# Kernel optimization log

Measured on AMD Instinct MI355X. Metric: run time of the kernel, lower is better.

The kernel has to match this reference:

```python
import math
import jax, jax.numpy as jnp
import numpy as np

V = 50257; D = 768; NL = 4; NH = 12; EXP = 4; FF = 4 * D; MAXS = 1024; ITERS = 10
HD = D // NH


def layernorm(x, g, b, eps=1e-5):
    mu = jnp.mean(x, axis=-1, keepdims=True)
    var = jnp.mean((x - mu) ** 2, axis=-1, keepdims=True)
    return (x - mu) * jax.lax.rsqrt(var + eps) * g + b


def sinkhorn(logM, iters=ITERS):
    # log-space Sinkhorn -> doubly-stochastic mixing matrix
    for _ in range(iters):
        logM = logM - jax.scipy.special.logsumexp(logM, axis=-1, keepdims=True)
        logM = logM - jax.scipy.special.logsumexp(logM, axis=-2, keepdims=True)
    return jnp.exp(logM)


def mhc(x, fn, W, b, alpha):
    # x: (B,S,n,D); dynamic manifold-constrained hyper-connection mixing
    B, S, n, d = x.shape
    xf = x.reshape(B, S, n * d)
    xn = xf * jax.lax.rsqrt(jnp.mean(xf * xf, axis=-1, keepdims=True) + 1e-6)
    logits = xn @ W * alpha + b                       # (B,S,n*n+2n)
    Hm = sinkhorn(logits[..., : n * n].reshape(B, S, n, n))
    pre = jax.nn.softmax(logits[..., n * n : n * n + n], axis=-1)   # (B,S,n)
    post = jax.nn.sigmoid(logits[..., n * n + n :])                 # (B,S,n)
    y = fn(jnp.einsum('bsn,bsnd->bsd', pre, x))                     # (B,S,D)
    return jnp.einsum('bsnm,bsmd->bsnd', Hm, x) + post[..., None] * y[:, :, None, :]


def attention(x, Wqkv, Wproj):
    B, S, _ = x.shape
    q, k, v = jnp.split(x @ Wqkv, 3, axis=-1)
    q = q.reshape(B, S, NH, HD).transpose(0, 2, 1, 3)
    k = k.reshape(B, S, NH, HD).transpose(0, 2, 1, 3)
    v = v.reshape(B, S, NH, HD).transpose(0, 2, 1, 3)
    scores = jnp.einsum('bhqd,bhkd->bhqk', q, k) * (1.0 / math.sqrt(HD))
    mask = jnp.tril(jnp.ones((S, S), dtype=bool))
    scores = jnp.where(mask, scores, -jnp.inf)
    attn = jax.nn.softmax(scores, axis=-1)
    o = jnp.einsum('bhqk,bhkd->bhqd', attn, v).transpose(0, 2, 1, 3).reshape(B, S, D)
    return o @ Wproj


def forward(input_ids, tok_emb, pos_emb, ln1_g, ln1_b, ln2_g, ln2_b,
            Wqkv, Wproj, Wfc1, Wfc2, mA_W, mA_b, mA_alpha,
            mF_W, mF_b, mF_alpha, lnf_g, lnf_b):
    B, S = input_ids.shape
    x = tok_emb[input_ids] + pos_emb[:S][None]          # (B,S,D)
    x = jnp.broadcast_to(x[:, :, None, :], (B, S, EXP, D))  # expand_to_mhc
    for l in range(NL):
        attn_fn = lambda h, l=l: attention(layernorm(h, ln1_g[l], ln1_b[l]), Wqkv[l], Wproj[l])
        x = mhc(x, attn_fn, mA_W[l], mA_b[l], mA_alpha[l])
        ffn_fn = lambda h, l=l: jax.nn.gelu(layernorm(h, ln2_g[l], ln2_b[l]) @ Wfc1[l], approximate=False) @ Wfc2[l]
        x = mhc(x, ffn_fn, mF_W[l], mF_b[l], mF_alpha[l])
    x = layernorm(jnp.sum(x, axis=2), lnf_g, lnf_b)     # contract_from_mhc + ln_f
    return x @ tok_emb.T                                # tied lm_head


def setup_inputs() -> dict:
    key = jax.random.key(0)
    ks = jax.random.split(key, 10)
    std = 0.02
    n2 = EXP * EXP + 2 * EXP
    return {
        'input_ids': jax.random.randint(ks[0], (2, 1024), 0, V),
        'tok_emb': std * jax.random.normal(ks[1], (V, D), jnp.float32),
        'pos_emb': std * jax.random.normal(ks[2], (MAXS, D), jnp.float32),
        'ln1_g': jnp.ones((NL, D)), 'ln1_b': jnp.zeros((NL, D)),
        'ln2_g': jnp.ones((NL, D)), 'ln2_b': jnp.zeros((NL, D)),
        'Wqkv': std * jax.random.normal(ks[3], (NL, D, 3 * D), jnp.float32),
        'Wproj': std * jax.random.normal(ks[4], (NL, D, D), jnp.float32),
        'Wfc1': std * jax.random.normal(ks[5], (NL, D, FF), jnp.float32),
        'Wfc2': std * jax.random.normal(ks[6], (NL, FF, D), jnp.float32),
        'mA_W': std * jax.random.normal(ks[7], (NL, EXP * D, n2), jnp.float32),
        'mA_b': jnp.zeros((NL, n2)),
        'mA_alpha': 0.01 * jnp.ones((NL,)),
        'mF_W': std * jax.random.normal(ks[8], (NL, EXP * D, n2), jnp.float32),
        'mF_b': jnp.zeros((NL, n2)),
        'mF_alpha': 0.01 * jnp.ones((NL,)),
        'lnf_g': jnp.ones((D,)), 'lnf_b': jnp.zeros((D,)),
    }


def reference(input_ids, tok_emb, pos_emb, ln1_g, ln1_b, ln2_g, ln2_b,
              Wqkv, Wproj, Wfc1, Wfc2, mA_W, mA_b, mA_alpha,
              mF_W, mF_b, mF_alpha, lnf_g, lnf_b):
    return forward(input_ids, tok_emb, pos_emb, ln1_g, ln1_b, ln2_g, ln2_b,
                   Wqkv, Wproj, Wfc1, Wfc2, mA_W, mA_b, mA_alpha,
                   mF_W, mF_b, mF_alpha, lnf_g, lnf_b)
```

## Files before the change

### kernel.cpp

```cpp
#include <hip/hip_runtime.h>
#include <math.h>

constexpr int BATCH  = 2;
constexpr int SEQ    = 1024;
constexpr int DIM    = 768;
constexpr int NLAYER = 4;
constexpr int NHEAD  = 12;
constexpr int HDIM   = 64;
constexpr int NEXP   = 4;
constexpr int FFDIM  = 3072;
constexpr int VOCAB  = 50257;
constexpr int NDIM   = NEXP * DIM;
constexpr int NC     = NEXP*NEXP + 2*NEXP;
constexpr int NTOK   = BATCH * SEQ;

using bf16x8 = __attribute__((ext_vector_type(8))) __bf16;
using f32x4  = __attribute__((ext_vector_type(4))) float;
using u16x8  = __attribute__((ext_vector_type(8))) unsigned short;

__device__ inline unsigned short f2bf(float f){
  unsigned u = __builtin_bit_cast(unsigned, f);
  u += 0x7fffu + ((u >> 16) & 1u);
  return (unsigned short)(u >> 16);
}
__device__ inline bf16x8 as_bf(u16x8 v){ return __builtin_bit_cast(bf16x8, v); }

constexpr size_t SZ_X   = (size_t)NTOK * NEXP * DIM;
constexpr size_t SZ_T   = (size_t)NTOK * DIM;
constexpr size_t O_X    = 0;
constexpr size_t O_X2   = O_X  + SZ_X;
constexpr size_t O_TMP  = O_X2 + SZ_X;
constexpr size_t O_BIG  = O_TMP + SZ_T;
constexpr size_t O_LNB  = O_BIG + (size_t)NTOK*2304;
constexpr size_t O_T1B  = O_LNB + SZ_T/2;
constexpr size_t O_COEF = O_T1B + SZ_T/2;
constexpr size_t O_WT   = O_COEF + (size_t)NTOK*NC;
constexpr size_t O_LNF  = 19298688;

__device__ inline float wred_sum(float v){
#pragma unroll
  for (int m=32;m>=1;m>>=1) v += __shfl_xor(v,m);
  return v;
}

template<bool FIRST>
__global__ __launch_bounds__(256) void k_mhc(const int* __restrict__ ids,
                                             const float* __restrict__ tokf,
                                             const float* __restrict__ posf,
                                             const float* __restrict__ xin,
                                             const float* __restrict__ y,
                                             float* __restrict__ xout,
                                             const float* __restrict__ W,
                                             const float* __restrict__ bb,
                                             const float* __restrict__ alpha_p,
                                             const float* __restrict__ g,
                                             const float* __restrict__ lnb_,
                                             float* __restrict__ coef,
                                             unsigned short* __restrict__ lnout){
  const int t = blockIdx.x, tid = threadIdx.x;
  const int w = tid >> 6;
  __shared__ float wred[4], w2[4];
  __shared__ float accw[4][NC];
  __shared__ float cfl[NC];

  float xp[3][4];
  float ss = 0.f;

  if constexpr (FIRST){
    const float* te = tokf + (size_t)ids[t]*DIM;
    const float* pe = posf + (size_t)(t % SEQ)*DIM;
#pragma unroll
    for (int k=0;k<3;k++){
      int d = tid + k*256;
      float v = te[d] + pe[d];
#pragma unroll
      for (int n=0;n<4;n++){
        xp[k][n] = v;
        xout[(size_t)t*NDIM + n*DIM + d] = v;
      }
      ss += 4.f*v*v;
    }
  } else {
    float cfp[20];
    const float* cp = coef + (size_t)t*NC;
#pragma unroll
    for (int j=0;j<16;j++) cfp[j] = cp[j];
#pragma unroll
    for (int j=0;j<4;j++) cfp[16+j] = cp[20+j];
    const float* xt = xin + (size_t)t*NDIM;
#pragma unroll
    for (int k=0;k<3;k++){
      int d = tid + k*256;
      float xm[4];
#pragma unroll
      for (int m=0;m<4;m++) xm[m] = xt[m*DIM + d];
      float yv = y[(size_t)t*DIM + d];
#pragma unroll
      for (int n=0;n<4;n++){
        float o = cfp[16+n]*yv;
#pragma unroll
        for (int m=0;m<4;m++) o += cfp[n*4+m]*xm[m];
        xp[k][n] = o;
        xout[(size_t)t*NDIM + n*DIM + d] = o;
        ss += o*o;
      }
    }
  }

  ss = wred_sum(ss);
  float acc[NC];
#pragma unroll
  for (int j=0;j<NC;j++) acc[j]=0.f;
#pragma unroll
  for (int k=0;k<3;k++){
    int d = tid + k*256;
#pragma unroll
    for (int n=0;n<4;n++){
      float v = xp[k][n];
      const float* wr = W + (size_t)(n*DIM + d)*NC;
#pragma unroll
      for (int j=0;j<NC;j++) acc[j] += v*wr[j];
    }
  }
#pragma unroll
  for (int j=0;j<NC;j++){
#pragma unroll
    for (int m=32;m>=1;m>>=1) acc[j] += __shfl_xor(acc[j], m);
  }
  if ((tid&63)==0){
    wred[w] = ss;
#pragma unroll
    for (int j=0;j<NC;j++) accw[w][j] = acc[j];
  }
  __syncthreads();
  float rfac = rsqrtf((wred[0]+wred[1]+wred[2]+wred[3])/(float)NDIM + 1e-6f);

  const float alpha = alpha_p[0];
  float* cfg = coef + (size_t)t*NC;
  if (tid < 16){
    float lmv = (accw[0][tid]+accw[1][tid]+accw[2][tid]+accw[3][tid])*rfac*alpha + bb[tid];
#pragma unroll
    for (int it=0; it<10; ++it){
      float mx = fmaxf(lmv, __shfl_xor(lmv,1)); mx = fmaxf(mx, __shfl_xor(mx,2));
      float se = expf(lmv-mx); se += __shfl_xor(se,1); se += __shfl_xor(se,2);
      lmv -= mx + logf(se);
      mx = fmaxf(lmv, __shfl_xor(lmv,4)); mx = fmaxf(mx, __shfl_xor(mx,8));
      se = expf(lmv-mx); se += __shfl_xor(se,4); se += __shfl_xor(se,8);
      lmv -= mx + logf(se);
    }
    float hm = expf(lmv);
    cfl[tid] = hm;
    cfg[tid] = hm;
  } else if (tid < 24){
    cfl[tid] = (accw[0][tid]+accw[1][tid]+accw[2][tid]+accw[3][tid])*rfac*alpha + bb[tid];
  }
  __syncthreads();
  if (tid == 0){
    float l0=cfl[16], l1=cfl[17], l2=cfl[18], l3=cfl[19];
    float pm = fmaxf(fmaxf(l0,l1),fmaxf(l2,l3));
    float e0=expf(l0-pm), e1=expf(l1-pm), e2=expf(l2-pm), e3=expf(l3-pm);
    float es=e0+e1+e2+e3;
    cfl[16]=e0/es; cfl[17]=e1/es; cfl[18]=e2/es; cfl[19]=e3/es;
#pragma unroll
    for (int j=20;j<24;j++) cfl[j] = 1.f/(1.f+expf(-cfl[j]));
#pragma unroll
    for (int j=16;j<24;j++) cfg[j] = cfl[j];
  }
  __syncthreads();

  float p0=cfl[16], p1=cfl[17], p2=cfl[18], p3=cfl[19];
  float h[3], s1=0.f, s2=0.f;
#pragma unroll
  for (int k=0;k<3;k++){
    float v = p0*xp[k][0] + p1*xp[k][1] + p2*xp[k][2] + p3*xp[k][3];
    h[k]=v; s1+=v; s2+=v*v;
  }
  s1 = wred_sum(s1); s2 = wred_sum(s2);
  if ((tid&63)==0){ wred[w]=s1; w2[w]=s2; }
  __syncthreads();
  float mu  = (wred[0]+wred[1]+wred[2]+wred[3])/(float)DIM;
  float var = (w2[0]+w2[1]+w2[2]+w2[3])/(float)DIM - mu*mu;
  float inv = rsqrtf(var + 1e-5f);
#pragma unroll
  for (int k=0;k<3;k++){
    int d = tid + k*256;
    lnout[(size_t)t*DIM+d] = f2bf((h[k]-mu)*inv*g[d] + lnb_[d]);
  }
}

__global__ __launch_bounds__(256) void k_csumln(const float* __restrict__ xin,
                                                const float* __restrict__ coef,
                                                const float* __restrict__ y,
                                                const float* __restrict__ g,
                                                const float* __restrict__ bb,
                                                unsigned short* __restrict__ out){
  const int t = blockIdx.x, tid = threadIdx.x;
  const int w = tid >> 6;
  const float* cp = coef + (size_t)t*NC;
  float cs[4];
#pragma unroll
  for (int m=0;m<4;m++) cs[m] = cp[m] + cp[4+m] + cp[8+m] + cp[12+m];
  float ps = cp[20]+cp[21]+cp[22]+cp[23];
  const float* xt = xin + (size_t)t*NDIM;
  float h[3], s1=0.f, s2=0.f;
#pragma unroll
  for (int k=0;k<3;k++){
    int d = tid + k*256;
    float v = ps * y[(size_t)t*DIM + d];
#pragma unroll
    for (int m=0;m<4;m++) v += cs[m]*xt[m*DIM + d];
    h[k]=v; s1+=v; s2+=v*v;
  }
  __shared__ float r1[4], r2[4];
  s1 = wred_sum(s1); s2 = wred_sum(s2);
  if ((tid&63)==0){ r1[w]=s1; r2[w]=s2; }
  __syncthreads();
  float mu  = (r1[0]+r1[1]+r1[2]+r1[3])/(float)DIM;
  float var = (r2[0]+r2[1]+r2[2]+r2[3])/(float)DIM - mu*mu;
  float inv = rsqrtf(var + 1e-5f);
#pragma unroll
  for (int k=0;k<3;k++){
    int d = tid + k*256;
    out[(size_t)t*DIM+d] = f2bf((h[k]-mu)*inv*g[d] + bb[d]);
  }
}

__global__ __launch_bounds__(256) void k_fattn(const unsigned short* __restrict__ qkv,
                                               unsigned short* __restrict__ out){
  const int qb = gridDim.x - 1 - blockIdx.x;
  const int h = blockIdx.y, b = blockIdx.z;
  const int tid = threadIdx.x;
  const int l = tid & 63, w = tid >> 6;
  const int lr = l & 15, lh = l >> 4;
  const int qw = qb*64 + w*16;
  constexpr int LDV = 68;
  __shared__ unsigned short Vt[64*LDV];
  __shared__ unsigned short Pl[4*16*LDV];
  unsigned short* Pw = Pl + w*16*LDV;

  const unsigned short* base = qkv + (size_t)b*SEQ*2304;

  u16x8 qa[2];
  {
    const unsigned short* qp = base + (size_t)(qw + lr)*2304 + h*64 + lh*8;
    qa[0] = *(const u16x8*)qp;
    qa[1] = *(const u16x8*)(qp + 32);
  }

  f32x4 o[4];
#pragma unroll
  for (int df=0; df<4; df++) o[df] = (f32x4){0.f,0.f,0.f,0.f};
  float m_run[4], l_run[4];
#pragma unroll
  for (int r=0;r<4;r++){ m_run[r] = -1e30f; l_run[r] = 0.f; }

  const int kTiles = qb + 1;
  for (int t=0; t<kTiles; ++t){
    const int k0 = t*64;
    __syncthreads();
#pragma unroll
    for (int i=0;i<2;i++){
      int f = tid + i*256;
      int k = f >> 3;
      int d0 = (f & 7) * 8;
      u16x8 v = *(const u16x8*)(base + (size_t)(k0+k)*2304 + 1536 + h*64 + d0);
#pragma unroll
      for (int j=0;j<8;j++) Vt[(d0+j)*LDV + k] = v[j];
    }
    __syncthreads();

    f32x4 s[4];
#pragma unroll
    for (int kf=0;kf<4;kf++) s[kf] = (f32x4){0.f,0.f,0.f,0.f};
#pragma unroll
    for (int ks=0;ks<2;ks++){
#pragma unroll
      for (int kf=0;kf<4;kf++){
        u16x8 kb = *(const u16x8*)(base + (size_t)(k0 + kf*16 + lr)*2304 + 768 + h*64 + ks*32 + lh*8);
        s[kf] = __builtin_amdgcn_mfma_f32_16x16x32_bf16(as_bf(qa[ks]), as_bf(kb), s[kf], 0,0,0);
      }
    }

    float sc[4][4];
#pragma unroll
    for (int kf=0;kf<4;kf++){
      int kg = k0 + kf*16 + lr;
#pragma unroll
      for (int r=0;r<4;r++){
        int qg = qw + lh*4 + r;
        sc[kf][r] = (kg <= qg) ? s[kf][r]*0.125f : -1e30f;
      }
    }
    float mt[4];
#pragma unroll
    for (int r=0;r<4;r++)
      mt[r] = fmaxf(fmaxf(sc[0][r],sc[1][r]), fmaxf(sc[2][r],sc[3][r]));
#pragma unroll
    for (int msk=1; msk<16; msk<<=1)
#pragma unroll
      for (int r=0;r<4;r++) mt[r] = fmaxf(mt[r], __shfl_xor(mt[r], msk));
    float c[4], rs[4];
#pragma unroll
    for (int r=0;r<4;r++){
      float mn = fmaxf(m_run[r], mt[r]);
      c[r] = expf(m_run[r] - mn);
      m_run[r] = mn;
      rs[r] = 0.f;
    }
#pragma unroll
    for (int kf=0;kf<4;kf++)
#pragma unroll
      for (int r=0;r<4;r++){
        float p = expf(sc[kf][r] - m_run[r]);
        rs[r] += p;
        Pw[(lh*4+r)*LDV + kf*16 + lr] = f2bf(p);
      }
#pragma unroll
    for (int msk=1; msk<16; msk<<=1)
#pragma unroll
      for (int r=0;r<4;r++) rs[r] += __shfl_xor(rs[r], msk);
#pragma unroll
    for (int r=0;r<4;r++) l_run[r] = l_run[r]*c[r] + rs[r];
#pragma unroll
    for (int df=0;df<4;df++)
#pragma unroll
      for (int r=0;r<4;r++) o[df][r] *= c[r];

#pragma unroll
    for (int ks=0;ks<2;ks++){
      u16x8 pa = *(const u16x8*)&Pw[lr*LDV + ks*32 + lh*8];
#pragma unroll
      for (int df=0;df<4;df++){
        u16x8 vb = *(const u16x8*)&Vt[(df*16 + lr)*LDV + ks*32 + lh*8];
        o[df] = __builtin_amdgcn_mfma_f32_16x16x32_bf16(as_bf(pa), as_bf(vb), o[df], 0,0,0);
      }
    }
  }

  float inv[4];
#pragma unroll
  for (int r=0;r<4;r++) inv[r] = 1.f/l_run[r];
#pragma unroll
  for (int df=0;df<4;df++)
#pragma unroll
    for (int r=0;r<4;r++){
      int qg = qw + lh*4 + r;
      out[((size_t)b*SEQ + qg)*DIM + h*64 + df*16 + lr] = f2bf(o[df][r]*inv[r]);
    }
}

__global__ __launch_bounds__(256) void k_wtrans4(const float* __restrict__ Wq, const float* __restrict__ Wp,
                                                 const float* __restrict__ W1, const float* __restrict__ W2,
                                                 unsigned short* __restrict__ dq, unsigned short* __restrict__ dp,
                                                 unsigned short* __restrict__ d1, unsigned short* __restrict__ d2){
  int bid = blockIdx.x;
  const float* src; unsigned short* dst; int K, N, local;
  if (bid < 1728)      { src=Wq; dst=dq; K=768;  N=2304; local=bid; }
  else if (bid < 2304) { src=Wp; dst=dp; K=768;  N=768;  local=bid-1728; }
  else if (bid < 4608) { src=W1; dst=d1; K=768;  N=3072; local=bid-2304; }
  else                 { src=W2; dst=d2; K=3072; N=768;  local=bid-4608; }
  int nx = N/32;
  int n0 = (local % nx)*32, k0 = (local / nx)*32;
  __shared__ float tile[32][33];
  int tx = threadIdx.x & 31, ty = threadIdx.x >> 5;
#pragma unroll
  for (int r=0;r<32;r+=8)
    tile[ty+r][tx] = src[(size_t)(k0+ty+r)*N + n0+tx];
  __syncthreads();
#pragma unroll
  for (int r=0;r<32;r+=8)
    dst[(size_t)(n0+ty+r)*K + k0+tx] = f2bf(tile[tx][ty+r]);
}

__global__ void k_cvt(const float* __restrict__ src, unsigned short* __restrict__ dst, int n8){
  int i = blockIdx.x*blockDim.x + threadIdx.x;
  for (; i < n8; i += gridDim.x*blockDim.x){
    float4 f0 = ((const float4*)src)[i*2];
    float4 f1 = ((const float4*)src)[i*2+1];
    u16x8 v;
    v[0]=f2bf(f0.x); v[1]=f2bf(f0.y); v[2]=f2bf(f0.z); v[3]=f2bf(f0.w);
    v[4]=f2bf(f1.x); v[5]=f2bf(f1.y); v[6]=f2bf(f1.z); v[7]=f2bf(f1.w);
    ((u16x8*)dst)[i] = v;
  }
}

template<int ACT, bool OUTBF, int BMT, int BNT, bool NT>
__global__ __launch_bounds__(256) void k_mgemm(const unsigned short* __restrict__ A,
                                               const unsigned short* __restrict__ B,
                                               void* __restrict__ Cout,
                                               int M, int N, int K)
{
  constexpr int MF = BMT/32;
  constexpr int NF = BNT/32;
  __shared__ __align__(16) unsigned short Sm[(BMT+BNT)*32];
  unsigned short* As = Sm;
  unsigned short* Bs = Sm + BMT*32;
  const int tid = threadIdx.x;
  const int l = tid & 63, w = tid >> 6;
  const int wr = w >> 1, wc = w & 1;

  const int nwg  = gridDim.x * gridDim.y;
  const int flat = blockIdx.y * gridDim.x + blockIdx.x;
  const int q8   = nwg >> 3;
  const int wk   = (flat & 7) * q8 + (flat >> 3);
  const int bm = (wk % gridDim.x) * BMT;
  const int bn = (wk / gridDim.x) * BNT;

  const int srow = tid >> 2;
  const int scol = (tid & 3) * 8;

  f32x4 acc[MF][NF];
#pragma unroll
  for (int i=0;i<MF;i++)
#pragma unroll
    for (int j=0;j<NF;j++) acc[i][j] = (f32x4){0.f,0.f,0.f,0.f};

  for (int k0 = 0; k0 < K; k0 += 32){
#pragma unroll
    for (int c=0;c<BMT/64;++c){
      const unsigned short* ga = A + (size_t)(bm + c*64 + srow)*K + (k0 + scol);
      __builtin_amdgcn_global_load_lds(
          (const __attribute__((address_space(1))) void*)ga,
          (__attribute__((address_space(3))) void*)(As + c*2048 + w*512),
          16, 0, 0);
    }
#pragma unroll
    for (int c=0;c<BNT/64;++c){
      int gn = bn + c*64 + srow; if (gn >= N) gn = N-1;
      const unsigned short* gb = B + (size_t)gn*K + (k0 + scol);
      __builtin_amdgcn_global_load_lds(
          (const __attribute__((address_space(1))) void*)gb,
          (__attribute__((address_space(3))) void*)(Bs + c*2048 + w*512),
          16, 0, 0);
    }
    __syncthreads();

    bf16x8 af[MF], bfr[NF];
#pragma unroll
    for (int i=0;i<MF;i++)
      af[i]  = *(const bf16x8*)(As + ((wr*(BMT/2) + i*16 + (l&15))*32 + (l>>4)*8));
#pragma unroll
    for (int j=0;j<NF;j++)
      bfr[j] = *(const bf16x8*)(Bs + ((wc*(BNT/2) + j*16 + (l&15))*32 + (l>>4)*8));
#pragma unroll
    for (int mi=0;mi<MF;mi++)
#pragma unroll
      for (int ni=0;ni<NF;ni++)
        acc[mi][ni] = __builtin_amdgcn_mfma_f32_16x16x32_bf16(af[mi], bfr[ni], acc[mi][ni], 0,0,0);
    __syncthreads();
  }

  if constexpr (OUTBF){
#pragma unroll
    for (int mi=0;mi<MF;mi++){
      const int gm0 = bm + wr*(BMT/2) + mi*16 + (l>>4)*4;
#pragma unroll
      for (int ni=0;ni<NF;ni++){
        const int gn = bn + wc*(BNT/2) + ni*16 + (l&15);
        if (gn < N){
#pragma unroll
          for (int r=0;r<4;r++){
            float v = acc[mi][ni][r];
            if constexpr (ACT==1) v = 0.5f*v*(1.f + erff(v*0.70710678118654752f));
            ((unsigned short*)Cout)[(size_t)(gm0+r)*N + gn] = f2bf(v);
          }
        }
      }
    }
  } else {
    float* band = (float*)Sm;
#pragma unroll
    for (int b=0; b<BMT/16; ++b){
      __syncthreads();
#pragma unroll
      for (int mi=0;mi<MF;mi++){
        if (b == wr*MF + mi){
#pragma unroll
          for (int ni=0;ni<NF;ni++){
#pragma unroll
            for (int r=0;r<4;r++){
              float v = acc[mi][ni][r];
              if constexpr (ACT==1) v = 0.5f*v*(1.f + erff(v*0.70710678118654752f));
              band[((l>>4)*4+r)*BNT + wc*(BNT/2) + ni*16 + (l&15)] = v;
            }
          }
        }
      }
      __syncthreads();
      const int row0 = bm + b*16;
#pragma unroll
      for (int p=0; p<(4*BNT)/256; ++p){
        int f = tid + p*256;
        int row = f/(BNT/4), c4 = f%(BNT/4);
        f32x4 v = *(const f32x4*)&band[row*BNT + c4*4];
        float* cp = (float*)Cout + (size_t)(row0+row)*N + bn + c4*4;
        if (bn + c4*4 + 3 < N){
          if constexpr (NT) __builtin_nontemporal_store(v, (f32x4*)cp);
          else *(f32x4*)cp = v;
        } else {
#pragma unroll
          for (int j=0;j<4;j++) if (bn + c4*4 + j < N) cp[j] = v[j];
        }
      }
    }
  }
}

extern "C" void kernel_launch(void* const* d_in, const int* in_sizes, int n_in,
                              void* d_out, int out_size, void* d_ws, size_t ws_size,
                              hipStream_t stream) {
  const int*   ids   = (const int*)  d_in[0];
  const float* tok   = (const float*)d_in[1];
  const float* pos   = (const float*)d_in[2];
  const float* ln1g  = (const float*)d_in[3];
  const float* ln1b  = (const float*)d_in[4];
  const float* ln2g  = (const float*)d_in[5];
  const float* ln2b  = (const float*)d_in[6];
  const float* Wqkv  = (const float*)d_in[7];
  const float* Wproj = (const float*)d_in[8];
  const float* Wfc1  = (const float*)d_in[9];
  const float* Wfc2  = (const float*)d_in[10];
  const float* mAW   = (const float*)d_in[11];
  const float* mAb   = (const float*)d_in[12];
  const float* mAal  = (const float*)d_in[13];
  const float* mFW   = (const float*)d_in[14];
  const float* mFb   = (const float*)d_in[15];
  const float* mFal  = (const float*)d_in[16];
  const float* lnfg  = (const float*)d_in[17];
  const float* lnfb  = (const float*)d_in[18];
  float* out = (float*)d_out;

  float* ws   = (float*)d_ws;
  float* xA   = ws + O_X;
  float* xB   = ws + O_X2;
  float* tmpF = ws + O_TMP;
  unsigned short* bigBF = (unsigned short*)(ws + O_BIG);
  unsigned short* lnbf  = (unsigned short*)(ws + O_LNB);
  unsigned short* t1bf  = (unsigned short*)(ws + O_T1B);
  float* coef = ws + O_COEF;
  unsigned short* wT    = (unsigned short*)(ws + O_WT);
  unsigned short* wqkvT  = wT;
  unsigned short* wprojT = wT + (size_t)2304*768;
  unsigned short* wfc1T  = wprojT + (size_t)768*768;
  unsigned short* wfc2T  = wfc1T + (size_t)3072*768;
  unsigned short* tokbf  = (unsigned short*)(ws + O_X);
  unsigned short* lnfbf  = (unsigned short*)(ws + O_LNF);

  float* xc = xA; float* xn = xB;
  for (int l=0; l<NLAYER; l++){
    k_wtrans4<<<6912, 256, 0, stream>>>(Wqkv + (size_t)l*DIM*3*DIM, Wproj + (size_t)l*DIM*DIM,
                                        Wfc1 + (size_t)l*DIM*FFDIM, Wfc2 + (size_t)l*FFDIM*DIM,
                                        wqkvT, wprojT, wfc1T, wfc2T);
    if (l == 0){
      k_mhc<true><<<NTOK, 256, 0, stream>>>(ids, tok, pos, nullptr, nullptr, xA,
                                            mAW, mAb, mAal, ln1g, ln1b, coef, lnbf);
    } else {
      k_mhc<false><<<NTOK, 256, 0, stream>>>(nullptr, nullptr, nullptr, xc, tmpF, xn,
                                             mAW + (size_t)l*NDIM*NC, mAb + (size_t)l*NC, mAal + l,
                                             ln1g + (size_t)l*DIM, ln1b + (size_t)l*DIM, coef, lnbf);
      { float* tmp = xc; xc = xn; xn = tmp; }
    }
    k_mgemm<0,true ,64,128,false><<<dim3(32, 2304/128), 256, 0, stream>>>(lnbf, wqkvT, (void*)bigBF, NTOK, 2304, 768);
    k_fattn<<<dim3(SEQ/64, NHEAD, BATCH), 256, 0, stream>>>(bigBF, t1bf);
    k_mgemm<0,false,64,64,false><<<dim3(32, 768/64), 256, 0, stream>>>(t1bf, wprojT, tmpF, NTOK, 768, 768);

    k_mhc<false><<<NTOK, 256, 0, stream>>>(nullptr, nullptr, nullptr, xc, tmpF, xn,
                                           mFW + (size_t)l*NDIM*NC, mFb + (size_t)l*NC, mFal + l,
                                           ln2g + (size_t)l*DIM, ln2b + (size_t)l*DIM, coef, lnbf);
    { float* tmp = xc; xc = xn; xn = tmp; }
    k_mgemm<1,true ,64,128,false><<<dim3(32, 3072/128), 256, 0, stream>>>(lnbf, wfc1T, (void*)bigBF, NTOK, 3072, 768);
    k_mgemm<0,false,64,64,false><<<dim3(32, 768/64), 256, 0, stream>>>(bigBF, wfc2T, tmpF, NTOK, 768, 3072);
  }

  k_csumln<<<NTOK, 256, 0, stream>>>(xc, coef, tmpF, lnfg, lnfb, lnfbf);
  k_cvt<<<2048, 256, 0, stream>>>(tok, tokbf, (VOCAB*DIM)/8);
  k_mgemm<0,false,128,128,true><<<dim3(16, (VOCAB+127)/128), 256, 0, stream>>>(lnfbf, tokbf, out, NTOK, VOCAB, 768);
}
```

Baseline: 1.729 ms.

## Transpose QK^T MFMA so softmax rows are lane-local, pass P via shuffles

The flash-attention kernel now computes S^T by swapping the MFMA operands, so each lane holds scores for a single query row. That collapses the max and sum reductions to two cross-lane shuffles and lets each lane keep scalar running statistics. The P tile is packed to bf16 and redistributed through register shuffles instead of a per-warp LDS buffer. V transpose stores are packed as 32-bit pairs, and expf is replaced with __expf. This trades LDS traffic and reduction shuffles for extra permute instructions and slightly looser exp accuracy.

```diff
diff --git a/kernel.cpp b/kernel.cpp
--- a/kernel.cpp
+++ b/kernel.cpp
@@ -17,6 +17,8 @@
 using bf16x8 = __attribute__((ext_vector_type(8))) __bf16;
 using f32x4  = __attribute__((ext_vector_type(4))) float;
 using u16x8  = __attribute__((ext_vector_type(8))) unsigned short;
+using u16x4  = __attribute__((ext_vector_type(4))) unsigned short;
+using u32x4  = __attribute__((ext_vector_type(4))) unsigned int;
 
 __device__ inline unsigned short f2bf(float f){
   unsigned u = __builtin_bit_cast(unsigned, f);
@@ -235,8 +237,6 @@
   const int qw = qb*64 + w*16;
   constexpr int LDV = 68;
   __shared__ unsigned short Vt[64*LDV];
-  __shared__ unsigned short Pl[4*16*LDV];
-  unsigned short* Pw = Pl + w*16*LDV;
 
   const unsigned short* base = qkv + (size_t)b*SEQ*2304;
 
@@ -250,22 +250,26 @@
   f32x4 o[4];
 #pragma unroll
   for (int df=0; df<4; df++) o[df] = (f32x4){0.f,0.f,0.f,0.f};
-  float m_run[4], l_run[4];
-#pragma unroll
-  for (int r=0;r<4;r++){ m_run[r] = -1e30f; l_run[r] = 0.f; }
+  float m_run = -1e30f, l_run = 0.f;
+  const int qg = qw + lr;
 
   const int kTiles = qb + 1;
   for (int t=0; t<kTiles; ++t){
     const int k0 = t*64;
     __syncthreads();
 #pragma unroll
-    for (int i=0;i<2;i++){
-      int f = tid + i*256;
-      int k = f >> 3;
-      int d0 = (f & 7) * 8;
-      u16x8 v = *(const u16x8*)(base + (size_t)(k0+k)*2304 + 1536 + h*64 + d0);
-#pragma unroll
-      for (int j=0;j<8;j++) Vt[(d0+j)*LDV + k] = v[j];
+    for (int p=0;p<2;p++){
+      int idx = p*256 + tid;
+      int k  = (idx >> 4) * 2;
+      int d0 = (idx & 15) * 4;
+      const unsigned short* vp = base + (size_t)(k0+k)*2304 + 1536 + h*64 + d0;
+      u16x4 v0 = *(const u16x4*)vp;
+      u16x4 v1 = *(const u16x4*)(vp + 2304);
+#pragma unroll
+      for (int j=0;j<4;j++){
+        unsigned pkv = (unsigned)v0[j] | ((unsigned)v1[j] << 16);
+        *(unsigned*)&Vt[(d0+j)*LDV + k] = pkv;
+      }
     }
     __syncthreads();
 
@@ -277,75 +281,88 @@
 #pragma unroll
       for (int kf=0;kf<4;kf++){
         u16x8 kb = *(const u16x8*)(base + (size_t)(k0 + kf*16 + lr)*2304 + 768 + h*64 + ks*32 + lh*8);
-        s[kf] = __builtin_amdgcn_mfma_f32_16x16x32_bf16(as_bf(qa[ks]), as_bf(kb), s[kf], 0,0,0);
+        s[kf] = __builtin_amdgcn_mfma_f32_16x16x32_bf16(as_bf(kb), as_bf(qa[ks]), s[kf], 0,0,0);
       }
     }
 
     float sc[4][4];
 #pragma unroll
     for (int kf=0;kf<4;kf++){
-      int kg = k0 + kf*16 + lr;
+      int kg0 = k0 + kf*16 + lh*4;
+#pragma unroll
+      for (int r=0;r<4;r++)
+        sc[kf][r] = (kg0 + r <= qg) ? s[kf][r]*0.125f : -1e30f;
+    }
+    float mt = sc[0][0];
+#pragma unroll
+    for (int kf=0;kf<4;kf++)
+#pragma unroll
+      for (int r=0;r<4;r++) mt = fmaxf(mt, sc[kf][r]);
+    mt = fmaxf(mt, __shfl_xor(mt, 16));
+    mt = fmaxf(mt, __shfl_xor(mt, 32));
+    float mn = fmaxf(m_run, mt);
+    float c  = __expf(m_run - mn);
+    m_run = mn;
+    float p[4][4];
+    float rs = 0.f;
+#pragma unroll
+    for (int kf=0;kf<4;kf++)
 #pragma unroll
       for (int r=0;r<4;r++){
-        int qg = qw + lh*4 + r;
-        sc[kf][r] = (kg <= qg) ? s[kf][r]*0.125f : -1e30f;
-      }
-    }
-    float mt[4];
-#pragma unroll
-    for (int r=0;r<4;r++)
-      mt[r] = fmaxf(fmaxf(sc[0][r],sc[1][r]), fmaxf(sc[2][r],sc[3][r]));
-#pragma unroll
-    for (int msk=1; msk<16; msk<<=1)
-#pragma unroll
-      for (int r=0;r<4;r++) mt[r] = fmaxf(mt[r], __shfl_xor(mt[r], msk));
-    float c[4], rs[4];
-#pragma unroll
-    for (int r=0;r<4;r++){
-      float mn = fmaxf(m_run[r], mt[r]);
-      c[r] = expf(m_run[r] - mn);
-      m_run[r] = mn;
-      rs[r] = 0.f;
-    }
-#pragma unroll
-    for (int kf=0;kf<4;kf++)
-#pragma unroll
-      for (int r=0;r<4;r++){
-        float p = expf(sc[kf][r] - m_run[r]);
-        rs[r] += p;
-        Pw[(lh*4+r)*LDV + kf*16 + lr] = f2bf(p);
-      }
-#pragma unroll
-    for (int msk=1; msk<16; msk<<=1)
-#pragma unroll
-      for (int r=0;r<4;r++) rs[r] += __shfl_xor(rs[r], msk);
-#pragma unroll
-    for (int r=0;r<4;r++) l_run[r] = l_run[r]*c[r] + rs[r];
+        float pv = __expf(sc[kf][r] - mn);
+        p[kf][r] = pv;
+        rs += pv;
+      }
+    rs += __shfl_xor(rs, 16);
+    rs += __shfl_xor(rs, 32);
+    l_run = l_run*c + rs;
+
+    float cq[4];
+#pragma unroll
+    for (int r=0;r<4;r++) cq[r] = __shfl(c, lh*4 + r);
 #pragma unroll
     for (int df=0;df<4;df++)
 #pragma unroll
-      for (int r=0;r<4;r++) o[df][r] *= c[r];
-
+      for (int r=0;r<4;r++) o[df][r] *= cq[r];
+
+    unsigned pk[4][2];
+#pragma unroll
+    for (int kf=0;kf<4;kf++){
+      pk[kf][0] = (unsigned)f2bf(p[kf][0]) | ((unsigned)f2bf(p[kf][1]) << 16);
+      pk[kf][1] = (unsigned)f2bf(p[kf][2]) | ((unsigned)f2bf(p[kf][3]) << 16);
+    }
+    const int srcA = lr + (lh&1)*32;
+    const int srcB = srcA + 16;
+    const bool hi = (lh>>1)&1;
 #pragma unroll
     for (int ks=0;ks<2;ks++){
-      u16x8 pa = *(const u16x8*)&Pw[lr*LDV + ks*32 + lh*8];
+      unsigned s00 = __shfl(pk[ks*2  ][0], srcA), s01 = __shfl(pk[ks*2  ][1], srcA);
+      unsigned s10 = __shfl(pk[ks*2+1][0], srcA), s11 = __shfl(pk[ks*2+1][1], srcA);
+      unsigned t00 = __shfl(pk[ks*2  ][0], srcB), t01 = __shfl(pk[ks*2  ][1], srcB);
+      unsigned t10 = __shfl(pk[ks*2+1][0], srcB), t11 = __shfl(pk[ks*2+1][1], srcB);
+      u32x4 paw;
+      paw[0] = hi ? s10 : s00;
+      paw[1] = hi ? s11 : s01;
+      paw[2] = hi ? t10 : t00;
+      paw[3] = hi ? t11 : t01;
+      bf16x8 pa = __builtin_bit_cast(bf16x8, paw);
 #pragma unroll
       for (int df=0;df<4;df++){
         u16x8 vb = *(const u16x8*)&Vt[(df*16 + lr)*LDV + ks*32 + lh*8];
-        o[df] = __builtin_amdgcn_mfma_f32_16x16x32_bf16(as_bf(pa), as_bf(vb), o[df], 0,0,0);
-      }
-    }
-  }
-
-  float inv[4];
-#pragma unroll
-  for (int r=0;r<4;r++) inv[r] = 1.f/l_run[r];
+        o[df] = __builtin_amdgcn_mfma_f32_16x16x32_bf16(pa, as_bf(vb), o[df], 0,0,0);
+      }
+    }
+  }
+
+  float linv[4];
+#pragma unroll
+  for (int r=0;r<4;r++) linv[r] = 1.f/__shfl(l_run, lh*4 + r);
 #pragma unroll
   for (int df=0;df<4;df++)
 #pragma unroll
     for (int r=0;r<4;r++){
-      int qg = qw + lh*4 + r;
-      out[((size_t)b*SEQ + qg)*DIM + h*64 + df*16 + lr] = f2bf(o[df][r]*inv[r]);
+      int qrow = qw + lh*4 + r;
+      out[((size_t)b*SEQ + qrow)*DIM + h*64 + df*16 + lr] = f2bf(o[df][r]*linv[r]);
     }
 }
 
```

Result: faster. 1.645 ms (-4.9%).
